# Performance work log

Hardware: AMD Instinct MI355X
Metric: run time of the kernel (lower is better)

## Reference

```python
import jax, jax.numpy as jnp
import numpy as np

N_NODES = 50000
N_EDGES = 800000
D = 128
N_LAYERS = 3


def setup_inputs() -> dict:
    key = jax.random.key(0)
    k = jax.random.split(key, 6)
    x = jax.random.normal(k[0], (N_NODES, D), dtype=jnp.float32)
    edge_index = jax.random.randint(k[1], (2, N_EDGES), 0, N_NODES, dtype=jnp.int64)
    scale = 1.0 / np.sqrt(D)
    # SAGEConv params per layer: lin_l (aggregated neighbors, with bias), lin_r (root)
    W_l = jax.random.uniform(k[2], (N_LAYERS, D, D), jnp.float32, -scale, scale)
    b_l = jax.random.uniform(k[3], (N_LAYERS, D), jnp.float32, -scale, scale)
    W_r = jax.random.uniform(k[4], (N_LAYERS, D, D), jnp.float32, -scale, scale)
    return {"x": x, "edge_index": edge_index, "W_l": W_l, "b_l": b_l, "W_r": W_r}


def _sage_layer(x, src, dst, inv_deg, Wl, bl, Wr):
    # gather source-node features, mean-aggregate into destination nodes
    msg = x[src]                                            # [E, D]
    agg = jax.ops.segment_sum(msg, dst, num_segments=N_NODES) * inv_deg  # [N, D]
    # out = lin_l(agg) + lin_r(x)
    return agg @ Wl.T + bl + x @ Wr.T


def reference(x, edge_index, W_l, b_l, W_r):
    src = edge_index[0]
    dst = edge_index[1]
    deg = jax.ops.segment_sum(jnp.ones((src.shape[0],), x.dtype), dst,
                              num_segments=N_NODES)
    inv_deg = (1.0 / jnp.maximum(deg, 1.0))[:, None]        # [N, 1]
    h = x
    for i in range(N_LAYERS):
        h = _sage_layer(h, src, dst, inv_deg, W_l[i], b_l[i], W_r[i])
        if i < N_LAYERS - 1:
            h = jax.nn.relu(h)  # dropout=0.0 -> identity
    return h
```

## Files before the change

### kernel.cpp

```cpp
#include <hip/hip_runtime.h>

#define N_NODES 50000
#define N_EDGES 800000
#define D 128
#define N_LAYERS 3
#define NBUCK ((N_NODES + 255) / 256)

typedef __attribute__((ext_vector_type(8))) short bfrag;
typedef __attribute__((ext_vector_type(4))) float f32x4;
typedef __attribute__((ext_vector_type(8))) unsigned short u16x8;

__device__ __forceinline__ unsigned short f2bf_rn(float f) {
    union { float f; unsigned u; } a; a.f = f;
    unsigned r = a.u + 0x7fffu + ((a.u >> 16) & 1u);
    return (unsigned short)(r >> 16);
}
__device__ __forceinline__ float bf2f(unsigned short h) {
    union { unsigned u; float f; } a; a.u = ((unsigned)h) << 16;
    return a.f;
}
__device__ __forceinline__ unsigned short f2h(float f) {
    union { unsigned short s[1]; _Float16 h; } a; a.h = (_Float16)f; return a.s[0];
}
__device__ __forceinline__ float h2f(unsigned short u) {
    union { unsigned short s[1]; _Float16 h; } a; a.s[0] = u; return (float)a.h;
}

#define GLOAD16(g, l) __builtin_amdgcn_global_load_lds( \
    (const __attribute__((address_space(1))) void*)(g), \
    (__attribute__((address_space(3))) void*)(l), 16, 0, 0)

__global__ void detect_dtype_kernel(const unsigned int* __restrict__ edge, int* __restrict__ flag,
                                    int* __restrict__ gcoarse) {
    __shared__ int any_nz;
    if (threadIdx.x == 0) any_nz = 0;
    __syncthreads();
    int nz = 0;
    for (int i = threadIdx.x; i < 2048; i += blockDim.x) {
        if (edge[2 * i + 1] != 0u) nz = 1;
    }
    if (nz) atomicOr(&any_nz, 1);
    for (int i = threadIdx.x; i < NBUCK; i += blockDim.x) gcoarse[i] = 0;
    __syncthreads();
    if (threadIdx.x == 0) *flag = any_nz ? 0 : 1;
}

__global__ __launch_bounds__(256) void hist_coarse_kernel(const int* __restrict__ edge,
                                                          const int* __restrict__ flag,
                                                          int* __restrict__ gcoarse) {
    __shared__ int h[NBUCK];
    const int t = threadIdx.x;
    for (int i = t; i < NBUCK; i += 256) h[i] = 0;
    __syncthreads();
    const int flagv = *flag;
    const int base = blockIdx.x * 1024;
#pragma unroll
    for (int j = 0; j < 4; ++j) {
        int i = base + j * 256 + t;
        if (i < N_EDGES) {
            int d = flagv ? edge[2 * ((size_t)N_EDGES + i)] : edge[N_EDGES + i];
            atomicAdd(&h[d >> 8], 1);
        }
    }
    __syncthreads();
    for (int i = t; i < NBUCK; i += 256)
        if (h[i]) atomicAdd(&gcoarse[i], h[i]);
}

__global__ __launch_bounds__(256) void scan196_kernel(const int* __restrict__ gcoarse,
                                                      int* __restrict__ bucket_base,
                                                      int* __restrict__ cursor1) {
    __shared__ int s[256];
    int t = threadIdx.x;
    int v = (t < NBUCK) ? gcoarse[t] : 0;
    s[t] = v;
    __syncthreads();
    for (int off = 1; off < 256; off <<= 1) {
        int u = (t >= off) ? s[t - off] : 0;
        __syncthreads();
        s[t] += u;
        __syncthreads();
    }
    if (t < NBUCK) {
        int excl = s[t] - v;
        bucket_base[t] = excl;
        cursor1[t] = excl;
    }
    if (t == 255) bucket_base[NBUCK] = s[255];
}

__global__ __launch_bounds__(256) void pass1_kernel(const int* __restrict__ edge,
                                                    const int* __restrict__ flag,
                                                    int* __restrict__ cursor1,
                                                    int* __restrict__ packed) {
    __shared__ int hist[NBUCK];
    __shared__ int base[NBUCK];
    const int t = threadIdx.x;
    const int flagv = *flag;
    const int blockBeg = blockIdx.x * 4096;
    for (int i = t; i < NBUCK; i += 256) hist[i] = 0;
    __syncthreads();
    int es[16], ed[16];
#pragma unroll
    for (int j = 0; j < 16; ++j) {
        int e = blockBeg + j * 256 + t;
        if (e < N_EDGES) {
            if (flagv) { es[j] = edge[2 * (size_t)e]; ed[j] = edge[2 * ((size_t)N_EDGES + e)]; }
            else       { es[j] = edge[e];             ed[j] = edge[N_EDGES + e]; }
        } else ed[j] = -1;
    }
#pragma unroll
    for (int j = 0; j < 16; ++j)
        if (ed[j] >= 0) atomicAdd(&hist[ed[j] >> 8], 1);
    __syncthreads();
    for (int i = t; i < NBUCK; i += 256) {
        base[i] = atomicAdd(&cursor1[i], hist[i]);
        hist[i] = 0;
    }
    __syncthreads();
#pragma unroll
    for (int j = 0; j < 16; ++j) {
        if (ed[j] >= 0) {
            int b = ed[j] >> 8;
            int pos = base[b] + atomicAdd(&hist[b], 1);
            packed[pos] = ((ed[j] & 255) << 18) | es[j];
        }
    }
}

__global__ __launch_bounds__(256) void build_csr_kernel(const int* __restrict__ bucket_base,
                                                        const int* __restrict__ packed,
                                                        int* __restrict__ offsets,
                                                        float* __restrict__ inv_deg,
                                                        int* __restrict__ csr) {
    __shared__ int cnt[256];
    __shared__ int s[256];
    const int t = threadIdx.x;
    const int b = blockIdx.x;
    const int base = bucket_base[b];
    const int endb = bucket_base[b + 1];
    cnt[t] = 0;
    __syncthreads();
    for (int e = base + t; e < endb; e += 256)
        atomicAdd(&cnt[((unsigned)packed[e]) >> 18], 1);
    __syncthreads();
    int v = cnt[t];
    s[t] = v;
    __syncthreads();
    for (int off = 1; off < 256; off <<= 1) {
        int u = (t >= off) ? s[t - off] : 0;
        __syncthreads();
        s[t] += u;
        __syncthreads();
    }
    int excl = base + s[t] - v;
    int node = b * 256 + t;
    if (node < N_NODES) {
        offsets[node] = excl;
        inv_deg[node] = 1.0f / (float)max(v, 1);
    }
    if (b == NBUCK - 1 && t == 0) offsets[N_NODES] = N_EDGES;
    cnt[t] = excl;
    __syncthreads();
    for (int e = base + t; e < endb; e += 256) {
        int p = packed[e];
        int pos = atomicAdd(&cnt[((unsigned)p) >> 18], 1);
        csr[pos] = p & 0x3FFFF;
    }
}

__global__ void prep_w_kernel(const float* __restrict__ Wl, const float* __restrict__ Wr,
                              unsigned short* __restrict__ WH, unsigned short* __restrict__ WL) {
    int idx = blockIdx.x * blockDim.x + threadIdx.x;
    if (idx >= N_LAYERS * 128 * 256) return;
    int k = idx & 255;
    int j = (idx >> 8) & 127;
    int l = idx >> 15;
    float v = (k < 128) ? Wl[((size_t)l * 128 + j) * 128 + k]
                        : Wr[((size_t)l * 128 + j) * 128 + (k - 128)];
    unsigned short hi = f2bf_rn(v);
    WH[idx] = hi;
    WL[idx] = f2bf_rn(v - bf2f(hi));
}

__global__ void split_x_kernel(const float* __restrict__ x, unsigned short* __restrict__ H16) {
    int t = blockIdx.x * 256 + threadIdx.x;
    if (t >= N_NODES * 32) return;
    float4 v = reinterpret_cast<const float4*>(x)[t];
    ushort4 h;
    h.x = f2h(v.x);
    h.y = f2h(v.y);
    h.z = f2h(v.z);
    h.w = f2h(v.w);
    reinterpret_cast<ushort4*>(H16)[t] = h;
}

__global__ __launch_bounds__(256) void aggregate_kernel(const unsigned short* __restrict__ hF16,
                                                        const int* __restrict__ offsets,
                                                        const int* __restrict__ csr_src,
                                                        const float* __restrict__ inv_deg,
                                                        unsigned short* __restrict__ aggH) {
    int node = blockIdx.x * 4 + (threadIdx.x >> 6);
    int lane = threadIdx.x & 63;
    int q = lane >> 4;
    int c = lane & 15;
    if (node >= N_NODES) return;
    int beg = offsets[node];
    int end = offsets[node + 1];
    float a0[8], a1[8];
#pragma unroll
    for (int j = 0; j < 8; ++j) { a0[j] = 0.f; a1[j] = 0.f; }
    int e = beg + q;
    for (; e + 4 < end; e += 8) {
        int s0 = csr_src[e];
        int s1 = csr_src[e + 4];
        u16x8 v0 = *reinterpret_cast<const u16x8*>(hF16 + (size_t)s0 * 128 + c * 8);
        u16x8 v1 = *reinterpret_cast<const u16x8*>(hF16 + (size_t)s1 * 128 + c * 8);
#pragma unroll
        for (int j = 0; j < 8; ++j) {
            a0[j] += h2f(v0[j]);
            a1[j] += h2f(v1[j]);
        }
    }
    if (e < end) {
        int s0 = csr_src[e];
        u16x8 v0 = *reinterpret_cast<const u16x8*>(hF16 + (size_t)s0 * 128 + c * 8);
#pragma unroll
        for (int j = 0; j < 8; ++j) a0[j] += h2f(v0[j]);
    }
#pragma unroll
    for (int j = 0; j < 8; ++j) a0[j] += a1[j];
#pragma unroll
    for (int j = 0; j < 8; ++j) a0[j] += __shfl_xor(a0[j], 16, 64);
#pragma unroll
    for (int j = 0; j < 8; ++j) a0[j] += __shfl_xor(a0[j], 32, 64);
    if (q == 0) {
        float w = inv_deg[node];
        u16x8 hi;
#pragma unroll
        for (int j = 0; j < 8; ++j) hi[j] = f2bf_rn(a0[j] * w);
        *reinterpret_cast<u16x8*>(aggH + (size_t)node * 128 + c * 8) = hi;
    }
}

template <int RELU, int LAST>
__global__ __launch_bounds__(256) void mfma_gemm_kernel(
    const unsigned short* __restrict__ aggH,
    const unsigned short* h16,
    const unsigned short* __restrict__ WH, const unsigned short* __restrict__ WL,
    const float* __restrict__ bias,
    float* __restrict__ OutF, unsigned short* H16o)
{
    __shared__ __align__(16) unsigned short Bh[4][128][8];
    __shared__ __align__(16) unsigned short Bl[4][128][8];
    const int tid = threadIdx.x;
    const int lane = tid & 63;
    const int wv = tid >> 6;
    const int m16 = lane & 15;
    const int kg = lane >> 4;
    const int blockRow = blockIdx.x * 64;
    const int rowg = blockRow + wv * 16 + m16;
    const int rowc = min(rowg, N_NODES - 1);

    f32x4 acc[8];
#pragma unroll
    for (int t = 0; t < 8; ++t) acc[t] = (f32x4){0.f, 0.f, 0.f, 0.f};

    for (int ks = 0; ks < 8; ++ks) {
        const int kc = ks * 32;
        bfrag a;
        if (ks < 4) {
            a = *reinterpret_cast<const bfrag*>(aggH + (size_t)rowc * 128 + kc + kg * 8);
        } else {
            u16x8 hv = *reinterpret_cast<const u16x8*>(h16 + (size_t)rowc * 128 + (kc - 128) + kg * 8);
#pragma unroll
            for (int j = 0; j < 8; ++j) a[j] = (short)f2bf_rn(h2f(hv[j]));
        }
        {
            const unsigned short* g0 = WH + (size_t)lane * 256 + kc + wv * 8;
            const unsigned short* g1 = WH + (size_t)(64 + lane) * 256 + kc + wv * 8;
            GLOAD16(g0, (char*)&Bh[0][0][0] + wv * 2048);
            GLOAD16(g1, (char*)&Bh[0][0][0] + wv * 2048 + 1024);
            const unsigned short* g2 = WL + (size_t)lane * 256 + kc + wv * 8;
            const unsigned short* g3 = WL + (size_t)(64 + lane) * 256 + kc + wv * 8;
            GLOAD16(g2, (char*)&Bl[0][0][0] + wv * 2048);
            GLOAD16(g3, (char*)&Bl[0][0][0] + wv * 2048 + 1024);
        }
        __syncthreads();
#pragma unroll
        for (int t = 0; t < 8; ++t) {
            bfrag bh = *reinterpret_cast<const bfrag*>(&Bh[kg][t * 16 + m16][0]);
            bfrag bl = *reinterpret_cast<const bfrag*>(&Bl[kg][t * 16 + m16][0]);
            acc[t] = __builtin_amdgcn_mfma_f32_16x16x32_bf16(a, bh, acc[t], 0, 0, 0);
            acc[t] = __builtin_amdgcn_mfma_f32_16x16x32_bf16(a, bl, acc[t], 0, 0, 0);
        }
        __syncthreads();
    }

#pragma unroll
    for (int t = 0; t < 8; ++t) {
        int col = t * 16 + m16;
        float bv = bias[col];
#pragma unroll
        for (int r = 0; r < 4; ++r) {
            int row = blockRow + wv * 16 + kg * 4 + r;
            if (row >= N_NODES) continue;
            float v = acc[t][r] + bv;
            if (RELU) v = fmaxf(v, 0.f);
            if (LAST) {
                OutF[(size_t)row * 128 + col] = v;
            } else {
                H16o[(size_t)row * 128 + col] = f2h(v);
            }
        }
    }
}

extern "C" void kernel_launch(void* const* d_in, const int* in_sizes, int n_in,
                              void* d_out, int out_size, void* d_ws, size_t ws_size,
                              hipStream_t stream) {
    const float* x  = (const float*)d_in[0];
    const int*   ei = (const int*)d_in[1];
    const float* Wl = (const float*)d_in[2];
    const float* bl = (const float*)d_in[3];
    const float* Wr = (const float*)d_in[4];
    float* out = (float*)d_out;
    char* ws = (char*)d_ws;

    int*            flag     = (int*)(ws + 0);
    int*            gcoarse  = (int*)(ws + 1024);
    int*            bbase    = (int*)(ws + 2048);
    int*            cursor1  = (int*)(ws + 3072);
    int*            offs     = (int*)(ws + 4096);
    float*          invd     = (float*)(ws + 208896);
    int*            packed   = (int*)(ws + 409600);
    int*            csr      = (int*)(ws + 3609600);
    unsigned short* WH       = (unsigned short*)(ws + 6809600);
    unsigned short* WL       = (unsigned short*)(ws + 7006208);
    unsigned short* h16      = (unsigned short*)(ws + 7202816);
    unsigned short* aggH     = (unsigned short*)(ws + 20002816);

    detect_dtype_kernel<<<1, 256, 0, stream>>>((const unsigned int*)ei, flag, gcoarse);
    hist_coarse_kernel<<<(N_EDGES + 1023) / 1024, 256, 0, stream>>>(ei, flag, gcoarse);
    scan196_kernel<<<1, 256, 0, stream>>>(gcoarse, bbase, cursor1);
    pass1_kernel<<<(N_EDGES + 4095) / 4096, 256, 0, stream>>>(ei, flag, cursor1, packed);
    build_csr_kernel<<<NBUCK, 256, 0, stream>>>(bbase, packed, offs, invd, csr);
    prep_w_kernel<<<(N_LAYERS * 128 * 256 + 255) / 256, 256, 0, stream>>>(Wl, Wr, WH, WL);
    split_x_kernel<<<(N_NODES * 32 + 255) / 256, 256, 0, stream>>>(x, h16);

    const int aggGrid = N_NODES / 4;
    const int gemmGrid = (N_NODES + 63) / 64;

    aggregate_kernel<<<aggGrid, 256, 0, stream>>>(h16, offs, csr, invd, aggH);
    mfma_gemm_kernel<1, 0><<<gemmGrid, 256, 0, stream>>>(aggH, h16,
        WH + 0 * 32768, WL + 0 * 32768, bl + 0, nullptr, h16);
    aggregate_kernel<<<aggGrid, 256, 0, stream>>>(h16, offs, csr, invd, aggH);
    mfma_gemm_kernel<1, 0><<<gemmGrid, 256, 0, stream>>>(aggH, h16,
        WH + 1 * 32768, WL + 1 * 32768, bl + 128, nullptr, h16);
    aggregate_kernel<<<aggGrid, 256, 0, stream>>>(h16, offs, csr, invd, aggH);
    mfma_gemm_kernel<0, 1><<<gemmGrid, 256, 0, stream>>>(aggH, h16,
        WH + 2 * 32768, WL + 2 * 32768, bl + 256, out, nullptr);
}
```

Measured before the change: 237.0 us.

## Fold bucket scan into consumer kernels and triple-buffer GEMM weight staging

Drops the single-block scan kernel. Each pass1 and build_csr block now recomputes the 196-entry prefix scan of the bucket counts in shared memory, so one launch and one serial dependency go away. The MFMA GEMM now triple-buffers weight tiles in LDS with async global-to-LDS loads and a vmcnt wait plus a single barrier per k-step, so the next tile's load overlaps the current MFMAs. The cost is redundant scan work in every block, three times the LDS use in the GEMM (which may lower occupancy), and reliance on hand-set waitcnt values being correct.

```diff
diff --git a/kernel.cpp b/kernel.cpp
--- a/kernel.cpp
+++ b/kernel.cpp
@@ -31,7 +31,7 @@
     (__attribute__((address_space(3))) void*)(l), 16, 0, 0)
 
 __global__ void detect_dtype_kernel(const unsigned int* __restrict__ edge, int* __restrict__ flag,
-                                    int* __restrict__ gcoarse) {
+                                    int* __restrict__ gcoarse, int* __restrict__ cursor1) {
     __shared__ int any_nz;
     if (threadIdx.x == 0) any_nz = 0;
     __syncthreads();
@@ -40,7 +40,7 @@
         if (edge[2 * i + 1] != 0u) nz = 1;
     }
     if (nz) atomicOr(&any_nz, 1);
-    for (int i = threadIdx.x; i < NBUCK; i += blockDim.x) gcoarse[i] = 0;
+    for (int i = threadIdx.x; i < NBUCK; i += blockDim.x) { gcoarse[i] = 0; cursor1[i] = 0; }
     __syncthreads();
     if (threadIdx.x == 0) *flag = any_nz ? 0 : 1;
 }
@@ -67,39 +67,30 @@
         if (h[i]) atomicAdd(&gcoarse[i], h[i]);
 }
 
-__global__ __launch_bounds__(256) void scan196_kernel(const int* __restrict__ gcoarse,
-                                                      int* __restrict__ bucket_base,
-                                                      int* __restrict__ cursor1) {
-    __shared__ int s[256];
-    int t = threadIdx.x;
-    int v = (t < NBUCK) ? gcoarse[t] : 0;
-    s[t] = v;
-    __syncthreads();
-    for (int off = 1; off < 256; off <<= 1) {
-        int u = (t >= off) ? s[t - off] : 0;
-        __syncthreads();
-        s[t] += u;
-        __syncthreads();
-    }
-    if (t < NBUCK) {
-        int excl = s[t] - v;
-        bucket_base[t] = excl;
-        cursor1[t] = excl;
-    }
-    if (t == 255) bucket_base[NBUCK] = s[255];
-}
-
 __global__ __launch_bounds__(256) void pass1_kernel(const int* __restrict__ edge,
                                                     const int* __restrict__ flag,
+                                                    const int* __restrict__ gcoarse,
                                                     int* __restrict__ cursor1,
                                                     int* __restrict__ packed) {
     __shared__ int hist[NBUCK];
+    __shared__ int lbase[256];
     __shared__ int base[NBUCK];
     const int t = threadIdx.x;
     const int flagv = *flag;
     const int blockBeg = blockIdx.x * 4096;
     for (int i = t; i < NBUCK; i += 256) hist[i] = 0;
-    __syncthreads();
+    {
+        int v = (t < NBUCK) ? gcoarse[t] : 0;
+        lbase[t] = v;
+        __syncthreads();
+        for (int off = 1; off < 256; off <<= 1) {
+            int u = (t >= off) ? lbase[t - off] : 0;
+            __syncthreads();
+            lbase[t] += u;
+            __syncthreads();
+        }
+        lbase[t] -= v;
+    }
     int es[16], ed[16];
 #pragma unroll
     for (int j = 0; j < 16; ++j) {
@@ -114,7 +105,7 @@
         if (ed[j] >= 0) atomicAdd(&hist[ed[j] >> 8], 1);
     __syncthreads();
     for (int i = t; i < NBUCK; i += 256) {
-        base[i] = atomicAdd(&cursor1[i], hist[i]);
+        base[i] = lbase[i] + atomicAdd(&cursor1[i], hist[i]);
         hist[i] = 0;
     }
     __syncthreads();
@@ -128,17 +119,29 @@
     }
 }
 
-__global__ __launch_bounds__(256) void build_csr_kernel(const int* __restrict__ bucket_base,
+__global__ __launch_bounds__(256) void build_csr_kernel(const int* __restrict__ gcoarse,
                                                         const int* __restrict__ packed,
                                                         int* __restrict__ offsets,
                                                         float* __restrict__ inv_deg,
                                                         int* __restrict__ csr) {
     __shared__ int cnt[256];
     __shared__ int s[256];
+    __shared__ int lbase[256];
     const int t = threadIdx.x;
     const int b = blockIdx.x;
-    const int base = bucket_base[b];
-    const int endb = bucket_base[b + 1];
+    {
+        int v = (t < NBUCK) ? gcoarse[t] : 0;
+        lbase[t] = v;
+        __syncthreads();
+        for (int off = 1; off < 256; off <<= 1) {
+            int u = (t >= off) ? lbase[t - off] : 0;
+            __syncthreads();
+            lbase[t] += u;
+            __syncthreads();
+        }
+    }
+    const int base = (b == 0) ? 0 : lbase[b - 1];
+    const int endb = lbase[b];
     cnt[t] = 0;
     __syncthreads();
     for (int e = base + t; e < endb; e += 256)
@@ -251,8 +254,7 @@
     const float* __restrict__ bias,
     float* __restrict__ OutF, unsigned short* H16o)
 {
-    __shared__ __align__(16) unsigned short Bh[4][128][8];
-    __shared__ __align__(16) unsigned short Bl[4][128][8];
+    __shared__ __align__(16) char smem[3 * 16384];
     const int tid = threadIdx.x;
     const int lane = tid & 63;
     const int wv = tid >> 6;
@@ -266,8 +268,20 @@
 #pragma unroll
     for (int t = 0; t < 8; ++t) acc[t] = (f32x4){0.f, 0.f, 0.f, 0.f};
 
+    auto stage = [&](int ks, int b) {
+        const int kc = ks * 32;
+        char* dst = smem + b * 16384 + wv * 2048;
+        GLOAD16(WH + (size_t)lane * 256 + kc + wv * 8, dst);
+        GLOAD16(WH + (size_t)(64 + lane) * 256 + kc + wv * 8, dst + 1024);
+        GLOAD16(WL + (size_t)lane * 256 + kc + wv * 8, dst + 8192);
+        GLOAD16(WL + (size_t)(64 + lane) * 256 + kc + wv * 8, dst + 8192 + 1024);
+    };
+
+    stage(0, 0);
+
     for (int ks = 0; ks < 8; ++ks) {
         const int kc = ks * 32;
+        const int cur = ks % 3;
         bfrag a;
         if (ks < 4) {
             a = *reinterpret_cast<const bfrag*>(aggH + (size_t)rowc * 128 + kc + kg * 8);
@@ -276,25 +290,23 @@
 #pragma unroll
             for (int j = 0; j < 8; ++j) a[j] = (short)f2bf_rn(h2f(hv[j]));
         }
-        {
-            const unsigned short* g0 = WH + (size_t)lane * 256 + kc + wv * 8;
-            const unsigned short* g1 = WH + (size_t)(64 + lane) * 256 + kc + wv * 8;
-            GLOAD16(g0, (char*)&Bh[0][0][0] + wv * 2048);
-            GLOAD16(g1, (char*)&Bh[0][0][0] + wv * 2048 + 1024);
-            const unsigned short* g2 = WL + (size_t)lane * 256 + kc + wv * 8;
-            const unsigned short* g3 = WL + (size_t)(64 + lane) * 256 + kc + wv * 8;
-            GLOAD16(g2, (char*)&Bl[0][0][0] + wv * 2048);
-            GLOAD16(g3, (char*)&Bl[0][0][0] + wv * 2048 + 1024);
-        }
-        __syncthreads();
+        if (ks < 7) {
+            stage(ks + 1, (ks + 1) % 3);
+            asm volatile("s_waitcnt vmcnt(4)" ::: "memory");
+        } else {
+            asm volatile("s_waitcnt vmcnt(0)" ::: "memory");
+        }
+        __builtin_amdgcn_s_barrier();
+        __builtin_amdgcn_sched_barrier(0);
+        const unsigned short* Bh = (const unsigned short*)(smem + cur * 16384 + kg * 2048);
+        const unsigned short* Bl = (const unsigned short*)(smem + cur * 16384 + 8192 + kg * 2048);
 #pragma unroll
         for (int t = 0; t < 8; ++t) {
-            bfrag bh = *reinterpret_cast<const bfrag*>(&Bh[kg][t * 16 + m16][0]);
-            bfrag bl = *reinterpret_cast<const bfrag*>(&Bl[kg][t * 16 + m16][0]);
+            bfrag bh = *reinterpret_cast<const bfrag*>(Bh + (t * 16 + m16) * 8);
+            bfrag bl = *reinterpret_cast<const bfrag*>(Bl + (t * 16 + m16) * 8);
             acc[t] = __builtin_amdgcn_mfma_f32_16x16x32_bf16(a, bh, acc[t], 0, 0, 0);
             acc[t] = __builtin_amdgcn_mfma_f32_16x16x32_bf16(a, bl, acc[t], 0, 0, 0);
         }
-        __syncthreads();
     }
 
 #pragma unroll
@@ -329,7 +341,6 @@
 
     int*            flag     = (int*)(ws + 0);
     int*            gcoarse  = (int*)(ws + 1024);
-    int*            bbase    = (int*)(ws + 2048);
     int*            cursor1  = (int*)(ws + 3072);
     int*            offs     = (int*)(ws + 4096);
     float*          invd     = (float*)(ws + 208896);
@@ -340,11 +351,10 @@
     unsigned short* h16      = (unsigned short*)(ws + 7202816);
     unsigned short* aggH     = (unsigned short*)(ws + 20002816);
 
-    detect_dtype_kernel<<<1, 256, 0, stream>>>((const unsigned int*)ei, flag, gcoarse);
+    detect_dtype_kernel<<<1, 256, 0, stream>>>((const unsigned int*)ei, flag, gcoarse, cursor1);
     hist_coarse_kernel<<<(N_EDGES + 1023) / 1024, 256, 0, stream>>>(ei, flag, gcoarse);
-    scan196_kernel<<<1, 256, 0, stream>>>(gcoarse, bbase, cursor1);
-    pass1_kernel<<<(N_EDGES + 4095) / 4096, 256, 0, stream>>>(ei, flag, cursor1, packed);
-    build_csr_kernel<<<NBUCK, 256, 0, stream>>>(bbase, packed, offs, invd, csr);
+    pass1_kernel<<<(N_EDGES + 4095) / 4096, 256, 0, stream>>>(ei, flag, gcoarse, cursor1, packed);
+    build_csr_kernel<<<NBUCK, 256, 0, stream>>>(gcoarse, packed, offs, invd, csr);
     prep_w_kernel<<<(N_LAYERS * 128 * 256 + 255) / 256, 256, 0, stream>>>(Wl, Wr, WH, WL);
     split_x_kernel<<<(N_NODES * 32 + 255) / 256, 256, 0, stream>>>(x, h16);
 
```

Result: slower. 251.6 us (+6.2%).
